# Kernel optimization log

Measured on AMD Instinct MI355X. Metric: run time of the kernel, lower is better.

## Reference

```python
import jax, jax.numpy as jnp
import numpy as np

N_EMBD = 1024
N_HEAD = 16
B, T = 4, 2048


def setup_inputs() -> dict:
    key = jax.random.key(0)
    ks = jax.random.split(key, 9)
    s = 1.0 / np.sqrt(N_EMBD)
    def lin(k):
        kw, kb = jax.random.split(k)
        W = jax.random.uniform(kw, (N_EMBD, N_EMBD), jnp.float32, -s, s)
        b = jax.random.uniform(kb, (N_EMBD,), jnp.float32, -s, s)
        return W, b
    Wq, bq = lin(ks[0])
    Wk, bk = lin(ks[1])
    Wv, bv = lin(ks[2])
    Wc, bc = lin(ks[3])
    x = jax.random.normal(ks[4], (B, T, N_EMBD), jnp.float32)
    return {"x": x, "Wq": Wq, "bq": bq, "Wk": Wk, "bk": bk,
            "Wv": Wv, "bv": bv, "Wc": Wc, "bc": bc}


def reference(x, Wq, bq, Wk, bk, Wv, bv, Wc, bc):
    Bsz, Tlen, C = x.shape
    hd = C // N_HEAD  # head dim
    # projections (torch Linear: x @ W.T + b)
    q = x @ Wq.T + bq
    k = x @ Wk.T + bk
    v = x @ Wv.T + bv
    # [B, H, T, hd]
    q = q.reshape(Bsz, Tlen, N_HEAD, hd).transpose(0, 2, 1, 3)
    k = k.reshape(Bsz, Tlen, N_HEAD, hd).transpose(0, 2, 1, 3)
    v = v.reshape(Bsz, Tlen, N_HEAD, hd).transpose(0, 2, 1, 3)
    scale = 1.0 / np.sqrt(hd).astype(np.float32)
    att = jnp.einsum('bhqd,bhkd->bhqk', q, k) * scale  # [B,H,T,T]
    causal = jnp.tril(jnp.ones((Tlen, Tlen), dtype=bool))
    att = jnp.where(causal[None, None, :, :], att, -jnp.inf)
    att = jax.nn.softmax(att, axis=-1)
    y = jnp.einsum('bhqk,bhkd->bhqd', att, v)  # [B,H,T,hd]
    y = y.transpose(0, 2, 1, 3).reshape(Bsz, Tlen, C)
    return y @ Wc.T + bc
```

## Files before the change

kernel.cpp:

```cpp
#include <hip/hip_runtime.h>
#include <hip/hip_bf16.h>

typedef __bf16 bf16x8 __attribute__((ext_vector_type(8)));
typedef float f32x4 __attribute__((ext_vector_type(4)));
typedef unsigned short u16;
typedef u16 u16x8 __attribute__((ext_vector_type(8)));
typedef unsigned int u32;
typedef u32 u32x4 __attribute__((ext_vector_type(4)));

#define N_EMBD 1024
#define NH 16
#define HD 64
#define BZ 4
#define TZ 2048
#define QSCALE 0.18033688011f

template<bool B> struct BoolC { static constexpr bool value = B; };

__device__ __forceinline__ u16 f2bf(float f) {
    return __builtin_bit_cast(u16, (__bf16)f);
}

__device__ __forceinline__ void gload16(const void* g, void* l) {
    __builtin_amdgcn_global_load_lds(
        (const __attribute__((address_space(1))) void*)g,
        (__attribute__((address_space(3))) void*)l, 16, 0, 0);
}

__global__ void cvt_all(const float* __restrict__ x,  const float* __restrict__ Wq,
                        const float* __restrict__ Wk, const float* __restrict__ Wv,
                        const float* __restrict__ Wc, u16* __restrict__ xb,
                        u16* __restrict__ wqkv, u16* __restrict__ wcb) {
    const int blk = blockIdx.x;
    const float* src; u16* dst; int base; float scale = 1.0f;
    if (blk < 8192)       { src = x;  dst = xb;             base = blk; }
    else if (blk < 9216)  { src = Wq; dst = wqkv;           base = blk - 8192; scale = QSCALE; }
    else if (blk < 10240) { src = Wk; dst = wqkv + 1048576; base = blk - 9216; }
    else if (blk < 11264) { src = Wv; dst = wqkv + 2097152; base = blk - 10240; }
    else                  { src = Wc; dst = wcb;            base = blk - 11264; }
    const int i = base * 256 + threadIdx.x;
    float4 f = ((const float4*)src)[i];
    ushort4 o;
    o.x = f2bf(f.x * scale); o.y = f2bf(f.y * scale);
    o.z = f2bf(f.z * scale); o.w = f2bf(f.w * scale);
    ((ushort4*)dst)[i] = o;
}

template<int EPI>
__global__ __launch_bounds__(512, 1) void gemm256_bt(
    const u16* __restrict__ A, const u16* __restrict__ Bm,
    const float* __restrict__ b0, const float* __restrict__ b1, const float* __restrict__ b2,
    void* __restrict__ Cout, int K) {
    __shared__ __align__(16) u16 Ash[4 * 8192];
    __shared__ __align__(16) u16 Bsh[4 * 8192];

    const int tid = threadIdx.x;
    const int lane = tid & 63, wid = tid >> 6;
    const int wm = wid >> 2, wn = wid & 3;
    const int m0 = blockIdx.x * 256, n0 = blockIdx.y * 256;
    const int r = lane & 15, g = lane >> 4;

    f32x4 acc[8][4] = {};

    const int p0 = tid >> 3;
    const int ci = tid & 7;
    const int cl = ci ^ (p0 & 7);
    const int trow = 2 * p0 + (cl >> 2);
    const int colb = (cl & 3) * 8;
    const u16* aS = A + (long)(m0 + trow) * K + colb;
    const u16* bS = Bm + (long)(n0 + trow) * K + colb;
    const long rowskip = (long)128 * K;
    const int ldst = tid * 8;

    auto STAGE = [&](int sig, int kq) {
        const u16* spA = aS + kq * 32;
        u16* dA = Ash + sig * 8192 + ldst;
        gload16(spA, dA);
        gload16(spA + rowskip, dA + 4096);
        const u16* spB = bS + kq * 32;
        u16* dB = Bsh + sig * 8192 + ldst;
        gload16(spB, dB);
        gload16(spB + rowskip, dB + 4096);
    };

    const int xa = (((((r & 1) << 2) | g) ^ (r >> 1)) << 4);
    const int arow0 = wm * 64 + (r >> 1);
    const int brow0 = wn * 32 + (r >> 1);
    auto RD = [&](const u16* base, int prow) -> bf16x8 {
        return *(const bf16x8*)((const char*)base + prow * 128 + xa);
    };

    const int nph = K >> 5;

    STAGE(0, 0); STAGE(1, 1);
    asm volatile("s_waitcnt vmcnt(4)" ::: "memory");
    __builtin_amdgcn_s_barrier();
    asm volatile("" ::: "memory");

#pragma unroll 1
    for (int p = 0; p < nph; ++p) {
        const int rho = p & 3, tgt = (p + 2) & 3;
        const int kq = (p + 2 < nph) ? p + 2 : 0;
        bf16x8 fa[8], fb[4];
        const u16* Ab = Ash + rho * 8192;
        const u16* Bb = Bsh + rho * 8192;
#pragma unroll
        for (int m = 0; m < 8; ++m) fa[m] = RD(Ab, arow0 + m * 8);
#pragma unroll
        for (int n = 0; n < 4; ++n) fb[n] = RD(Bb, brow0 + n * 8);
        STAGE(tgt, kq);
        asm volatile("" ::: "memory");
        __builtin_amdgcn_s_barrier();
        asm volatile("s_waitcnt lgkmcnt(0)" ::: "memory");
        __builtin_amdgcn_sched_barrier(0);
        __builtin_amdgcn_s_setprio(1);
#pragma unroll
        for (int m = 0; m < 8; ++m)
#pragma unroll
            for (int n = 0; n < 4; ++n)
                acc[m][n] = __builtin_amdgcn_mfma_f32_16x16x32_bf16(fa[m], fb[n], acc[m][n], 0, 0, 0);
        __builtin_amdgcn_s_setprio(0);
        asm volatile("s_waitcnt vmcnt(4)" ::: "memory");
        asm volatile("" ::: "memory");
        __builtin_amdgcn_s_barrier();
        asm volatile("" ::: "memory");
    }
    asm volatile("s_waitcnt vmcnt(0)" ::: "memory");

    const long planeSz = (long)BZ * NH * TZ * HD;
    if constexpr (EPI == 0) {
        const int proj = n0 >> 10;
        u16* outp = (u16*)Cout;
        if (proj == 2) {
            const int bi = (m0 + wm * 128) >> 11;
#pragma unroll
            for (int n = 0; n < 4; ++n) {
                const int rr = (n0 & 1023) + wn * 64 + n * 16 + r;
                const int h = rr >> 6, d = rr & 63;
                const float bias = b2[rr];
                u16* vcol = outp + 2 * planeSz + (((long)bi * NH + h) * HD + d) * TZ;
#pragma unroll
                for (int mf = 0; mf < 8; ++mf) {
                    const int t0 = (m0 + wm * 128 + mf * 16 + g * 4) & 2047;
                    ushort4 o;
                    o.x = f2bf(acc[mf][n][0] + bias);
                    o.y = f2bf(acc[mf][n][1] + bias);
                    o.z = f2bf(acc[mf][n][2] + bias);
                    o.w = f2bf(acc[mf][n][3] + bias);
                    *(ushort4*)(vcol + t0) = o;
                }
            }
        } else {
#pragma unroll
            for (int n = 0; n < 4; ++n) {
                const int rr = (n0 & 1023) + wn * 64 + n * 16 + r;
                const int h = rr >> 6, d = rr & 63;
                float bias = (proj == 0 ? b0 : b1)[rr];
                if (proj == 0) bias *= QSCALE;
                const long pbase = (long)proj * planeSz + d;
#pragma unroll
                for (int mf = 0; mf < 8; ++mf)
#pragma unroll
                    for (int reg = 0; reg < 4; ++reg) {
                        const int row = m0 + wm * 128 + mf * 16 + g * 4 + reg;
                        const int bi = row >> 11, t = row & 2047;
                        outp[pbase + ((long)bi * NH + h) * (TZ * HD) + (long)t * HD] =
                            f2bf(acc[mf][n][reg] + bias);
                    }
            }
        }
    } else {
        float* outp = (float*)Cout;
#pragma unroll
        for (int n = 0; n < 4; ++n) {
            const int col = n0 + wn * 64 + n * 16 + r;
            const float bias = b0[col];
#pragma unroll
            for (int mf = 0; mf < 8; ++mf)
#pragma unroll
                for (int reg = 0; reg < 4; ++reg) {
                    const int row = m0 + wm * 128 + mf * 16 + g * 4 + reg;
                    outp[(long)row * N_EMBD + col] = acc[mf][n][reg] + bias;
                }
        }
    }
}

template<int EPI>
__global__ __launch_bounds__(512, 2) void gemm_bt(
    const u16* __restrict__ A, const u16* __restrict__ Bm,
    const float* __restrict__ b0, const float* __restrict__ b1, const float* __restrict__ b2,
    void* __restrict__ Cout, int K) {
    __shared__ __align__(16) u16 Ash[6 * 8192];
    __shared__ __align__(16) u16 Bsh[6 * 4096];

    const int tid = threadIdx.x;
    const int lane = tid & 63, wid = tid >> 6;
    const int wm = wid >> 1, wn = wid & 1;
    const int m0 = blockIdx.x * 256, n0 = blockIdx.y * 128;
    const int r = lane & 15, g = lane >> 4;

    f32x4 acc[4][4] = {};

    const int p0 = tid >> 3;
    const int ci = tid & 7;
    const int cl = ci ^ (p0 & 7);
    const int trow = 2 * p0 + (cl >> 2);
    const int colb = (cl & 3) * 8;
    const u16* aS = A + (long)(m0 + trow) * K + colb;
    const u16* bS = Bm + (long)(n0 + trow) * K + colb;
    const long rowskip = (long)128 * K;
    const int ldst = tid * 8;

    auto STAGE = [&](int sig, int kq) {
        const u16* spA = aS + kq * 32;
        gload16(spA, &Ash[sig * 8192 + ldst]);
        gload16(spA + rowskip, &Ash[sig * 8192 + 4096 + ldst]);
        gload16(bS + kq * 32, &Bsh[sig * 4096 + ldst]);
    };

    const int xa = (((((r & 1) << 2) | g) ^ (r >> 1)) << 4);
    const int arow0 = wm * 32 + (r >> 1);
    const int brow0 = wn * 32 + (r >> 1);
    auto RD = [&](const u16* base, int prow) -> bf16x8 {
        return *(const bf16x8*)((const char*)base + prow * 128 + xa);
    };

    bf16x8 fa0[4], fb0[4], fa1[4], fb1[4];

    auto READF = [&](int rho, bf16x8* fa, bf16x8* fb) {
#pragma unroll
        for (int m = 0; m < 4; ++m) fa[m] = RD(&Ash[rho * 8192], arow0 + m * 8);
#pragma unroll
        for (int n = 0; n < 4; ++n) fb[n] = RD(&Bsh[rho * 4096], brow0 + n * 8);
    };
    auto MM = [&](bf16x8* fa, bf16x8* fb) {
        __builtin_amdgcn_s_setprio(1);
#pragma unroll
        for (int m = 0; m < 4; ++m)
#pragma unroll
            for (int n = 0; n < 4; ++n)
                acc[m][n] = __builtin_amdgcn_mfma_f32_16x16x32_bf16(fa[m], fb[n], acc[m][n], 0, 0, 0);
        __builtin_amdgcn_s_setprio(0);
    };
    auto BAR = [&] {
        asm volatile("" ::: "memory");
        __builtin_amdgcn_s_barrier();
        asm volatile("" ::: "memory");
    };

    const int nph = K >> 5;

    STAGE(0, 0); STAGE(1, 1); STAGE(2, 2); STAGE(3, 3); STAGE(4, 4);
    asm volatile("s_waitcnt vmcnt(9)" ::: "memory");
    BAR();
    READF(0, fa0, fb0);

    int rho = 0;
    for (int p = 0; p + 2 < nph; p += 2) {
        const int rho1 = rho + 1;
        const int rho2 = (rho + 2 == 6) ? 0 : rho + 2;
        const int sigE = (rho == 0) ? 5 : rho - 1;
        const int kqE = (p + 5 < nph) ? p + 5 : 0;
        const int kqO = (p + 6 < nph) ? p + 6 : 0;
        BAR();
        READF(rho1, fa1, fb1);
        STAGE(sigE, kqE);
        MM(fa0, fb0);
        asm volatile("s_waitcnt vmcnt(9)" ::: "memory");
        BAR();
        READF(rho2, fa0, fb0);
        STAGE(rho, kqO);
        MM(fa1, fb1);
        asm volatile("s_waitcnt vmcnt(9)" ::: "memory");
        rho = rho2;
    }
    {
        const int rho1 = rho + 1;
        const int sigE = (rho == 0) ? 5 : rho - 1;
        BAR();
        READF(rho1, fa1, fb1);
        STAGE(sigE, 0);
        MM(fa0, fb0);
        asm volatile("s_waitcnt vmcnt(9)" ::: "memory");
    }
    MM(fa1, fb1);
    asm volatile("s_waitcnt vmcnt(0)" ::: "memory");

    const long planeSz = (long)BZ * NH * TZ * HD;
    if constexpr (EPI == 0) {
        const int proj = n0 >> 10;
        u16* outp = (u16*)Cout;
        if (proj == 2) {
            const int bi = (m0 + wm * 64) >> 11;
#pragma unroll
            for (int n = 0; n < 4; ++n) {
                const int rr = (n0 & 1023) + wn * 64 + n * 16 + r;
                const int h = rr >> 6, d = rr & 63;
                const float bias = b2[rr];
                u16* vcol = outp + 2 * planeSz + (((long)bi * NH + h) * HD + d) * TZ;
#pragma unroll
                for (int m = 0; m < 4; ++m) {
                    const int t0 = (m0 + wm * 64 + m * 16 + g * 4) & 2047;
                    ushort4 o;
                    o.x = f2bf(acc[m][n][0] + bias);
                    o.y = f2bf(acc[m][n][1] + bias);
                    o.z = f2bf(acc[m][n][2] + bias);
                    o.w = f2bf(acc[m][n][3] + bias);
                    *(ushort4*)(vcol + t0) = o;
                }
            }
        } else {
#pragma unroll
            for (int n = 0; n < 4; ++n) {
                const int rr = (n0 & 1023) + wn * 64 + n * 16 + r;
                const int h = rr >> 6, d = rr & 63;
                float bias = (proj == 0 ? b0 : b1)[rr];
                if (proj == 0) bias *= QSCALE;
                const long pbase = (long)proj * planeSz + d;
#pragma unroll
                for (int m = 0; m < 4; ++m)
#pragma unroll
                    for (int reg = 0; reg < 4; ++reg) {
                        const int row = m0 + wm * 64 + m * 16 + g * 4 + reg;
                        const int bi = row >> 11, t = row & 2047;
                        outp[pbase + ((long)bi * NH + h) * (TZ * HD) + (long)t * HD] =
                            f2bf(acc[m][n][reg] + bias);
                    }
            }
        }
    } else {
        float* outp = (float*)Cout;
#pragma unroll
        for (int n = 0; n < 4; ++n) {
            const int col = n0 + wn * 64 + n * 16 + r;
            const float bias = b0[col];
#pragma unroll
            for (int m = 0; m < 4; ++m)
#pragma unroll
                for (int reg = 0; reg < 4; ++reg) {
                    const int row = m0 + wm * 64 + m * 16 + g * 4 + reg;
                    outp[(long)row * N_EMBD + col] = acc[m][n][reg] + bias;
                }
        }
    }
}

__device__ __forceinline__ bf16x8 lds_swz8(const u16* base, int row, int colByte) {
    return *(const bf16x8*)((const char*)base + row * 128 + (colByte ^ ((row & 7) << 4)));
}

__global__ __launch_bounds__(512, 2) void attn_fwd(const u16* __restrict__ qkv, u16* __restrict__ yb) {
    const int i = blockIdx.x;
    const int xcd = i & 7, slot = i >> 3;
    const int bh = xcd + 8 * (slot & 7);
    const int pr = slot >> 3;
    const int b = bh >> 4, h = bh & 15;
    const int tid = threadIdx.x, lane = tid & 63, w = tid >> 6;
    const int r = lane & 15, g = lane >> 4;

    __shared__ __align__(16) u16 Ksh[2][64 * 64];
    __shared__ __align__(16) u16 Vsh[2][64 * 64];

    const long planeSz = (long)BZ * NH * TZ * HD;
    const long bhoff = ((long)b * NH + h) * (long)TZ * HD;
    const u16* qp = qkv + bhoff;
    const u16* kp = qkv + planeSz + bhoff;
    const u16* vTp = qkv + 2 * planeSz + bhoff;

    const int rr8 = tid >> 3;
    const int ss = ((tid & 7) ^ (rr8 & 7)) * 8;

#pragma unroll 1
    for (int it = 0; it < 2; ++it) {
        const int qblk = it ? pr : (15 - pr);
        const int q0 = qblk * 128;
        const int nkt = 2 * qblk + 2;

        bf16x8 qf[2];
        {
            const int q = q0 + w * 16 + r;
#pragma unroll
            for (int ks = 0; ks < 2; ++ks)
                qf[ks] = *(const bf16x8*)(qp + (long)q * HD + ks * 32 + g * 8);
        }

        f32x4 yacc[4] = {};
        float mrun = -__builtin_inff(), lpart = 0.f;

        gload16(kp + (long)rr8 * HD + ss, &Ksh[0][tid * 8]);
        gload16(vTp + (long)rr8 * TZ + ss, &Vsh[0][tid * 8]);

        auto tile = [&](int kt, auto maskc) {
            constexpr bool MASK = decltype(maskc)::value;
            const int cur = kt & 1;
            const int k0 = kt * 64;
            if (kt + 1 < nkt) {
                const int k0n = k0 + 64;
                gload16(kp + (long)(k0n + rr8) * HD + ss, &Ksh[cur ^ 1][tid * 8]);
                gload16(vTp + (long)rr8 * TZ + k0n + ss, &Vsh[cur ^ 1][tid * 8]);
                asm volatile("s_waitcnt vmcnt(2)" ::: "memory");
            } else {
                asm volatile("s_waitcnt vmcnt(0)" ::: "memory");
            }
            __builtin_amdgcn_s_barrier();
            asm volatile("" ::: "memory");

            f32x4 sac[4] = {};
#pragma unroll
            for (int ks = 0; ks < 2; ++ks) {
                bf16x8 kf[4];
#pragma unroll
                for (int nk = 0; nk < 4; ++nk)
                    kf[nk] = lds_swz8(Ksh[cur], nk * 16 + r, ks * 64 + g * 16);
                __builtin_amdgcn_s_setprio(1);
#pragma unroll
                for (int nk = 0; nk < 4; ++nk)
                    sac[nk] = __builtin_amdgcn_mfma_f32_16x16x32_bf16(kf[nk], qf[ks], sac[nk], 0, 0, 0);
                __builtin_amdgcn_s_setprio(0);
            }

            if constexpr (MASK) {
                const int q = q0 + w * 16 + r;
#pragma unroll
                for (int nk = 0; nk < 4; ++nk)
#pragma unroll
                    for (int reg = 0; reg < 4; ++reg) {
                        const int k = k0 + nk * 16 + g * 4 + reg;
                        sac[nk][reg] = (k > q) ? -__builtin_inff() : sac[nk][reg];
                    }
            }
            float pmax;
            {
                float t0 = fmaxf(fmaxf(sac[0][0], sac[0][1]), fmaxf(sac[0][2], sac[0][3]));
                float t1 = fmaxf(fmaxf(sac[1][0], sac[1][1]), fmaxf(sac[1][2], sac[1][3]));
                float t2 = fmaxf(fmaxf(sac[2][0], sac[2][1]), fmaxf(sac[2][2], sac[2][3]));
                float t3 = fmaxf(fmaxf(sac[3][0], sac[3][1]), fmaxf(sac[3][2], sac[3][3]));
                pmax = fmaxf(fmaxf(t0, t1), fmaxf(t2, t3));
            }
            if (__any(pmax > mrun + 8.0f)) {
                float mx = pmax;
                mx = fmaxf(mx, __shfl_xor(mx, 16));
                mx = fmaxf(mx, __shfl_xor(mx, 32));
                const float mnew = fmaxf(mrun, mx);
                const float corr = __builtin_amdgcn_exp2f(mrun - mnew);
                lpart *= corr;
#pragma unroll
                for (int nd = 0; nd < 4; ++nd)
                    yacc[nd] *= corr;
                mrun = mnew;
            }
            float rs[4];
#pragma unroll
            for (int nk = 0; nk < 4; ++nk) {
                float p0 = __builtin_amdgcn_exp2f(sac[nk][0] - mrun);
                float p1 = __builtin_amdgcn_exp2f(sac[nk][1] - mrun);
                float p2 = __builtin_amdgcn_exp2f(sac[nk][2] - mrun);
                float p3 = __builtin_amdgcn_exp2f(sac[nk][3] - mrun);
                sac[nk][0] = p0; sac[nk][1] = p1;
                sac[nk][2] = p2; sac[nk][3] = p3;
                rs[nk] = (p0 + p1) + (p2 + p3);
            }
            lpart += (rs[0] + rs[1]) + (rs[2] + rs[3]);

            u32 wv[4][2];
#pragma unroll
            for (int nk = 0; nk < 4; ++nk)
#pragma unroll
                for (int j2 = 0; j2 < 2; ++j2)
                    asm("v_cvt_pk_bf16_f32 %0, %1, %2"
                        : "=v"(wv[nk][j2])
                        : "v"(sac[nk][2 * j2]), "v"(sac[nk][2 * j2 + 1]));
            u32 pw[2][4];
#pragma unroll
            for (int ks = 0; ks < 2; ++ks) {
                u32 a0 = wv[2 * ks][0], b0 = wv[2 * ks + 1][0];
                u32 a1 = wv[2 * ks][1], b1 = wv[2 * ks + 1][1];
                asm("v_permlane32_swap_b32 %0, %1" : "+v"(a0), "+v"(b0));
                asm("v_permlane32_swap_b32 %0, %1" : "+v"(a1), "+v"(b1));
                asm("v_permlane16_swap_b32 %0, %1" : "+v"(a0), "+v"(b0));
                asm("v_permlane16_swap_b32 %0, %1" : "+v"(a1), "+v"(b1));
                pw[ks][0] = a0; pw[ks][1] = a1;
                pw[ks][2] = b0; pw[ks][3] = b1;
            }

#pragma unroll
            for (int ks = 0; ks < 2; ++ks) {
                bf16x8 vf[4];
#pragma unroll
                for (int nd = 0; nd < 4; ++nd)
                    vf[nd] = lds_swz8(Vsh[cur], nd * 16 + r, ks * 64 + g * 16);
                const u32x4 pwv = { pw[ks][0], pw[ks][1], pw[ks][2], pw[ks][3] };
                const bf16x8 pb = __builtin_bit_cast(bf16x8, pwv);
                __builtin_amdgcn_s_setprio(1);
#pragma unroll
                for (int nd = 0; nd < 4; ++nd)
                    yacc[nd] = __builtin_amdgcn_mfma_f32_16x16x32_bf16(vf[nd], pb, yacc[nd], 0, 0, 0);
                __builtin_amdgcn_s_setprio(0);
            }

            asm volatile("" ::: "memory");
            __builtin_amdgcn_s_barrier();
            asm volatile("" ::: "memory");
        };

        for (int kt = 0; kt + 2 < nkt; ++kt) tile(kt, BoolC<false>{});
        tile(nkt - 2, BoolC<true>{});
        tile(nkt - 1, BoolC<true>{});

        {
            float l = lpart;
            l += __shfl_xor(l, 16);
            l += __shfl_xor(l, 32);
            const float inv = 1.f / l;
            const int q = q0 + w * 16 + r;
            u16* orow = yb + ((long)b * TZ + q) * N_EMBD + h * HD;
#pragma unroll
            for (int nd = 0; nd < 4; ++nd) {
                ushort4 o;
                o.x = f2bf(yacc[nd][0] * inv);
                o.y = f2bf(yacc[nd][1] * inv);
                o.z = f2bf(yacc[nd][2] * inv);
                o.w = f2bf(yacc[nd][3] * inv);
                *(ushort4*)(orow + nd * 16 + g * 4) = o;
            }
        }
    }
}

extern "C" void kernel_launch(void* const* d_in, const int* in_sizes, int n_in,
                              void* d_out, int out_size, void* d_ws, size_t ws_size,
                              hipStream_t stream) {
    const float* x  = (const float*)d_in[0];
    const float* Wq = (const float*)d_in[1];
    const float* bq = (const float*)d_in[2];
    const float* Wk = (const float*)d_in[3];
    const float* bk = (const float*)d_in[4];
    const float* Wv = (const float*)d_in[5];
    const float* bv = (const float*)d_in[6];
    const float* Wc = (const float*)d_in[7];
    const float* bc = (const float*)d_in[8];

    char* ws = (char*)d_ws;
    u16* xb   = (u16*)(ws);
    u16* wqkv = (u16*)(ws + 16777216);
    u16* wcb  = (u16*)(ws + 23068672);
    u16* qkv  = (u16*)(ws + 25165824);
    u16* yb   = (u16*)(ws + 75497472);

    cvt_all<<<12288, 256, 0, stream>>>(x, Wq, Wk, Wv, Wc, xb, wqkv, wcb);

    gemm256_bt<0><<<dim3(32, 12), 512, 0, stream>>>(xb, wqkv, bq, bk, bv, (void*)qkv, 1024);

    attn_fwd<<<512, 512, 0, stream>>>(qkv, yb);

    gemm_bt<1><<<dim3(32, 8), 512, 0, stream>>>(yb, wcb, bc, nullptr, nullptr, d_out, 1024);
}
```

Before: 168.9 us.

## Retile QKV GEMM to 16 waves with register double-buffered fragments; hoist V reads

The QKV projection GEMM now runs 1024 threads per block. Each of the 16 waves computes a 64x64 sub-tile instead of 128x64. The main loop is restructured into a software pipeline: LDS prefetch runs three stages ahead, and register fragments are double-buffered so LDS reads for the next k-step overlap the current MFMAs. In attention, the V fragments are loaded from LDS before the QK^T and softmax work to hide LDS latency. The new __launch_bounds__(1024, 4) asks for more occupancy than the 128KB LDS footprint allows, which may squeeze the register budget and cause spills.

Result: slower. 309.0 us (+82.9%).

```diff
diff --git a/kernel.cpp b/kernel.cpp
--- a/kernel.cpp
+++ b/kernel.cpp
@@ -47,7 +47,7 @@
 }
 
 template<int EPI>
-__global__ __launch_bounds__(512, 1) void gemm256_bt(
+__global__ __launch_bounds__(1024, 4) void gemm256_bt(
     const u16* __restrict__ A, const u16* __restrict__ Bm,
     const float* __restrict__ b0, const float* __restrict__ b1, const float* __restrict__ b2,
     void* __restrict__ Cout, int K) {
@@ -60,7 +60,7 @@
     const int m0 = blockIdx.x * 256, n0 = blockIdx.y * 256;
     const int r = lane & 15, g = lane >> 4;
 
-    f32x4 acc[8][4] = {};
+    f32x4 acc[4][4] = {};
 
     const int p0 = tid >> 3;
     const int ci = tid & 7;
@@ -69,62 +69,75 @@
     const int colb = (cl & 3) * 8;
     const u16* aS = A + (long)(m0 + trow) * K + colb;
     const u16* bS = Bm + (long)(n0 + trow) * K + colb;
-    const long rowskip = (long)128 * K;
     const int ldst = tid * 8;
 
     auto STAGE = [&](int sig, int kq) {
-        const u16* spA = aS + kq * 32;
-        u16* dA = Ash + sig * 8192 + ldst;
-        gload16(spA, dA);
-        gload16(spA + rowskip, dA + 4096);
-        const u16* spB = bS + kq * 32;
-        u16* dB = Bsh + sig * 8192 + ldst;
-        gload16(spB, dB);
-        gload16(spB + rowskip, dB + 4096);
+        gload16(aS + kq * 32, &Ash[sig * 8192 + ldst]);
+        gload16(bS + kq * 32, &Bsh[sig * 8192 + ldst]);
     };
 
     const int xa = (((((r & 1) << 2) | g) ^ (r >> 1)) << 4);
-    const int arow0 = wm * 64 + (r >> 1);
+    const int arow0 = wm * 32 + (r >> 1);
     const int brow0 = wn * 32 + (r >> 1);
     auto RD = [&](const u16* base, int prow) -> bf16x8 {
         return *(const bf16x8*)((const char*)base + prow * 128 + xa);
     };
 
-    const int nph = K >> 5;
-
-    STAGE(0, 0); STAGE(1, 1);
-    asm volatile("s_waitcnt vmcnt(4)" ::: "memory");
-    __builtin_amdgcn_s_barrier();
-    asm volatile("" ::: "memory");
-
-#pragma unroll 1
-    for (int p = 0; p < nph; ++p) {
-        const int rho = p & 3, tgt = (p + 2) & 3;
-        const int kq = (p + 2 < nph) ? p + 2 : 0;
-        bf16x8 fa[8], fb[4];
-        const u16* Ab = Ash + rho * 8192;
-        const u16* Bb = Bsh + rho * 8192;
-#pragma unroll
-        for (int m = 0; m < 8; ++m) fa[m] = RD(Ab, arow0 + m * 8);
-#pragma unroll
-        for (int n = 0; n < 4; ++n) fb[n] = RD(Bb, brow0 + n * 8);
-        STAGE(tgt, kq);
-        asm volatile("" ::: "memory");
-        __builtin_amdgcn_s_barrier();
-        asm volatile("s_waitcnt lgkmcnt(0)" ::: "memory");
-        __builtin_amdgcn_sched_barrier(0);
+    bf16x8 fa0[4], fb0[4], fa1[4], fb1[4];
+
+    auto READF = [&](int rho, bf16x8* fa, bf16x8* fb) {
+#pragma unroll
+        for (int m = 0; m < 4; ++m) fa[m] = RD(&Ash[rho * 8192], arow0 + m * 8);
+#pragma unroll
+        for (int n = 0; n < 4; ++n) fb[n] = RD(&Bsh[rho * 8192], brow0 + n * 8);
+    };
+    auto MM = [&](bf16x8* fa, bf16x8* fb) {
         __builtin_amdgcn_s_setprio(1);
 #pragma unroll
-        for (int m = 0; m < 8; ++m)
+        for (int m = 0; m < 4; ++m)
 #pragma unroll
             for (int n = 0; n < 4; ++n)
                 acc[m][n] = __builtin_amdgcn_mfma_f32_16x16x32_bf16(fa[m], fb[n], acc[m][n], 0, 0, 0);
         __builtin_amdgcn_s_setprio(0);
-        asm volatile("s_waitcnt vmcnt(4)" ::: "memory");
+    };
+    auto BAR = [&] {
         asm volatile("" ::: "memory");
         __builtin_amdgcn_s_barrier();
         asm volatile("" ::: "memory");
-    }
+    };
+
+    const int nph = K >> 5;
+
+    STAGE(0, 0); STAGE(1, 1); STAGE(2, 2);
+    asm volatile("s_waitcnt vmcnt(4)" ::: "memory");
+    BAR();
+    READF(0, fa0, fb0);
+
+    int rho = 0;
+    for (int p = 0; p + 2 < nph; p += 2) {
+        const int rho1 = (rho + 1) & 3;
+        const int rho2 = (rho + 2) & 3;
+        const int kqE = (p + 3 < nph) ? p + 3 : 0;
+        const int kqO = (p + 4 < nph) ? p + 4 : 0;
+        BAR();
+        READF(rho1, fa1, fb1);
+        STAGE((rho + 3) & 3, kqE);
+        MM(fa0, fb0);
+        asm volatile("s_waitcnt vmcnt(2)" ::: "memory");
+        BAR();
+        READF(rho2, fa0, fb0);
+        STAGE(rho, kqO);
+        MM(fa1, fb1);
+        asm volatile("s_waitcnt vmcnt(2)" ::: "memory");
+        rho = rho2;
+    }
+    {
+        const int rho1 = (rho + 1) & 3;
+        BAR();
+        READF(rho1, fa1, fb1);
+        MM(fa0, fb0);
+    }
+    MM(fa1, fb1);
     asm volatile("s_waitcnt vmcnt(0)" ::: "memory");
 
     const long planeSz = (long)BZ * NH * TZ * HD;
@@ -132,7 +145,7 @@
         const int proj = n0 >> 10;
         u16* outp = (u16*)Cout;
         if (proj == 2) {
-            const int bi = (m0 + wm * 128) >> 11;
+            const int bi = (m0 + wm * 64) >> 11;
 #pragma unroll
             for (int n = 0; n < 4; ++n) {
                 const int rr = (n0 & 1023) + wn * 64 + n * 16 + r;
@@ -140,13 +153,13 @@
                 const float bias = b2[rr];
                 u16* vcol = outp + 2 * planeSz + (((long)bi * NH + h) * HD + d) * TZ;
 #pragma unroll
-                for (int mf = 0; mf < 8; ++mf) {
-                    const int t0 = (m0 + wm * 128 + mf * 16 + g * 4) & 2047;
+                for (int m = 0; m < 4; ++m) {
+                    const int t0 = (m0 + wm * 64 + m * 16 + g * 4) & 2047;
                     ushort4 o;
-                    o.x = f2bf(acc[mf][n][0] + bias);
-                    o.y = f2bf(acc[mf][n][1] + bias);
-                    o.z = f2bf(acc[mf][n][2] + bias);
-                    o.w = f2bf(acc[mf][n][3] + bias);
+                    o.x = f2bf(acc[m][n][0] + bias);
+                    o.y = f2bf(acc[m][n][1] + bias);
+                    o.z = f2bf(acc[m][n][2] + bias);
+                    o.w = f2bf(acc[m][n][3] + bias);
                     *(ushort4*)(vcol + t0) = o;
                 }
             }
@@ -159,13 +172,13 @@
                 if (proj == 0) bias *= QSCALE;
                 const long pbase = (long)proj * planeSz + d;
 #pragma unroll
-                for (int mf = 0; mf < 8; ++mf)
+                for (int m = 0; m < 4; ++m)
 #pragma unroll
                     for (int reg = 0; reg < 4; ++reg) {
-                        const int row = m0 + wm * 128 + mf * 16 + g * 4 + reg;
+                        const int row = m0 + wm * 64 + m * 16 + g * 4 + reg;
                         const int bi = row >> 11, t = row & 2047;
                         outp[pbase + ((long)bi * NH + h) * (TZ * HD) + (long)t * HD] =
-                            f2bf(acc[mf][n][reg] + bias);
+                            f2bf(acc[m][n][reg] + bias);
                     }
             }
         }
@@ -176,11 +189,11 @@
             const int col = n0 + wn * 64 + n * 16 + r;
             const float bias = b0[col];
 #pragma unroll
-            for (int mf = 0; mf < 8; ++mf)
+            for (int m = 0; m < 4; ++m)
 #pragma unroll
                 for (int reg = 0; reg < 4; ++reg) {
-                    const int row = m0 + wm * 128 + mf * 16 + g * 4 + reg;
-                    outp[(long)row * N_EMBD + col] = acc[mf][n][reg] + bias;
+                    const int row = m0 + wm * 64 + m * 16 + g * 4 + reg;
+                    outp[(long)row * N_EMBD + col] = acc[m][n][reg] + bias;
                 }
         }
     }
@@ -406,6 +419,13 @@
             __builtin_amdgcn_s_barrier();
             asm volatile("" ::: "memory");
 
+            bf16x8 vf[2][4];
+#pragma unroll
+            for (int ks = 0; ks < 2; ++ks)
+#pragma unroll
+                for (int nd = 0; nd < 4; ++nd)
+                    vf[ks][nd] = lds_swz8(Vsh[cur], nd * 16 + r, ks * 64 + g * 16);
+
             f32x4 sac[4] = {};
 #pragma unroll
             for (int ks = 0; ks < 2; ++ks) {
@@ -486,16 +506,12 @@
 
 #pragma unroll
             for (int ks = 0; ks < 2; ++ks) {
-                bf16x8 vf[4];
-#pragma unroll
-                for (int nd = 0; nd < 4; ++nd)
-                    vf[nd] = lds_swz8(Vsh[cur], nd * 16 + r, ks * 64 + g * 16);
                 const u32x4 pwv = { pw[ks][0], pw[ks][1], pw[ks][2], pw[ks][3] };
                 const bf16x8 pb = __builtin_bit_cast(bf16x8, pwv);
                 __builtin_amdgcn_s_setprio(1);
 #pragma unroll
                 for (int nd = 0; nd < 4; ++nd)
-                    yacc[nd] = __builtin_amdgcn_mfma_f32_16x16x32_bf16(vf[nd], pb, yacc[nd], 0, 0, 0);
+                    yacc[nd] = __builtin_amdgcn_mfma_f32_16x16x32_bf16(vf[ks][nd], pb, yacc[nd], 0, 0, 0);
                 __builtin_amdgcn_s_setprio(0);
             }
 
@@ -550,7 +566,7 @@
 
     cvt_all<<<12288, 256, 0, stream>>>(x, Wq, Wk, Wv, Wc, xb, wqkv, wcb);
 
-    gemm256_bt<0><<<dim3(32, 12), 512, 0, stream>>>(xb, wqkv, bq, bk, bv, (void*)qkv, 1024);
+    gemm256_bt<0><<<dim3(32, 12), 1024, 0, stream>>>(xb, wqkv, bq, bk, bv, (void*)qkv, 1024);
 
     attn_fwd<<<512, 512, 0, stream>>>(qkv, yb);
 
```
